# Kernel optimization log

Measured on AMD Instinct MI355X. Metric: run time of the kernel, lower is better.

## Reference

```python
import jax, jax.numpy as jnp
import numpy as np

EMBED_DIM = 1024
NUM_HEADS = 16
HEAD_DIM = EMBED_DIM // NUM_HEADS
SCALE = HEAD_DIM ** -0.5
B, N = 2, 2048


def setup_inputs() -> dict:
    key = jax.random.key(0)
    ks = jax.random.split(key, 18)
    s = 1.0 / np.sqrt(EMBED_DIM)
    inp = {
        'x': jax.random.normal(ks[0], (B, N, EMBED_DIM), jnp.float32),
        'context': jax.random.normal(ks[1], (B, N, EMBED_DIM), jnp.float32),
    }
    names = ['q', 'k', 'v', 'o', 'cq', 'ck', 'cv']
    for i, nm in enumerate(names):
        inp['W' + nm] = jax.random.normal(ks[2 + 2 * i], (EMBED_DIM, EMBED_DIM), jnp.float32) * s
        inp['b' + nm] = jax.random.normal(ks[3 + 2 * i], (EMBED_DIM,), jnp.float32) * s
    return inp


def _linear(x, W, b):
    # torch nn.Linear: x @ W.T + b, W is [out, in]
    return jnp.einsum('bnc,oc->bno', x, W) + b


def reference(x, context, Wq, bq, Wk, bk, Wv, bv, Wo, bo, Wcq, bcq, Wck, bck, Wcv, bcv):
    Bsz, Nseq, C = x.shape
    # self-attention with head split
    def split(t):
        return t.reshape(Bsz, Nseq, NUM_HEADS, HEAD_DIM).transpose(0, 2, 1, 3)  # [B,H,N,D]
    q = split(_linear(x, Wq, bq))
    k = split(_linear(x, Wk, bk))
    v = split(_linear(x, Wv, bv))
    scores = jnp.einsum('bhnd,bhmd->bhnm', q, k) * SCALE  # [B,H,N,N]
    attn = jax.nn.softmax(scores, axis=-1)  # dropout is identity in eval
    out = jnp.einsum('bhnm,bhmd->bhnd', attn, v)
    out = out.transpose(0, 2, 1, 3).reshape(Bsz, Nseq, C)
    attn_output = _linear(out, Wo, bo)
    # cross-attention branch: NO head split (faithful to original)
    cq = _linear(attn_output, Wcq, bcq)  # [B,N,C]
    ck = _linear(context, Wck, bck)      # [B,M,C]
    cv = _linear(context, Wcv, bcv)      # [B,M,C]
    cscores = jnp.einsum('bnc,bmc->bnm', cq, ck) * SCALE  # [B,N,M]
    cattn = jax.nn.softmax(cscores, axis=-1)
    cross_out = jnp.einsum('bnm,bmc->bnc', cattn, cv)
    return attn_output + cross_out
```

## Files before the change

kernel.cpp:

```cpp
#include <hip/hip_runtime.h>
#include <stdint.h>

typedef __attribute__((ext_vector_type(8))) short short8;
typedef __attribute__((ext_vector_type(4))) float f32x4;
typedef unsigned short u16;
typedef unsigned int u32;

#define SCALE 0.125f

__device__ __forceinline__ u16 f2bf(float f) {
  u32 u = __builtin_bit_cast(u32, f);
  u32 r = (u + 0x7FFFu + ((u >> 16) & 1u)) >> 16;
  return (u16)r;
}
__device__ __forceinline__ u16 f2bf_fast(float f) {
  return (u16)((__builtin_bit_cast(u32, f) + 0x8000u) >> 16);
}
__device__ __forceinline__ float bf2f(u16 h) {
  u32 u = ((u32)h) << 16;
  return __builtin_bit_cast(float, u);
}

__device__ __forceinline__ void gload16(const void* g, void* l) {
  __builtin_amdgcn_global_load_lds(
      (const __attribute__((address_space(1))) u32*)g,
      (__attribute__((address_space(3))) u32*)l, 16, 0, 0);
}

#define MFMA16(a, b, c) __builtin_amdgcn_mfma_f32_16x16x32_bf16((a), (b), (c), 0, 0, 0)

__global__ void fill_f32(float* __restrict__ p, float v, int n) {
  int i = blockIdx.x * 256 + threadIdx.x;
  if (i < n) p[i] = v;
}

__global__ void cvt_f32_bf16_s(const float* __restrict__ src, u16* __restrict__ dst,
                               int n, float s) {
  int i = (blockIdx.x * 256 + threadIdx.x) * 4;
  if (i >= n) return;
  float4 v = *(const float4*)(src + i);
  u32* d = (u32*)(dst + i);
  d[0] = (u32)f2bf(v.x * s) | ((u32)f2bf(v.y * s) << 16);
  d[1] = (u32)f2bf(v.z * s) | ((u32)f2bf(v.w * s) << 16);
}

__global__ void copy_scale_f32(const float* __restrict__ s, float* __restrict__ d,
                               int n, float sc) {
  int i = blockIdx.x * 256 + threadIdx.x;
  if (i < n) d[i] = s[i] * sc;
}

template <int MODE>
__global__ __launch_bounds__(512) void gemm_nt(
    const u16* __restrict__ A, int64_t lda, int64_t sAz,
    const u16* __restrict__ B, int64_t ldb, int64_t sBz,
    void* __restrict__ Cv, int64_t ldc, int64_t sCz, u16* __restrict__ C2,
    const float* __restrict__ bias, const float* __restrict__ biasR,
    float alpha, int K)
{
  __shared__ u16 sA[128 * 64];
  __shared__ u16 sB[128 * 64];
  const int tid = threadIdx.x;
  const int lane = tid & 63, w = tid >> 6, g = lane >> 4, c = lane & 15;
  const int wr = w >> 1, wc = w & 1;
  const int64_t m0 = (int64_t)blockIdx.y * 128, n0 = (int64_t)blockIdx.x * 128;
  A += (int64_t)blockIdx.z * sAz;
  B += (int64_t)blockIdx.z * sBz;

  f32x4 acc[2][4] = {};

  int sL[2];
  const u16* gA[2];
  const u16* gB[2];
#pragma unroll
  for (int i = 0; i < 2; ++i) {
    int s = tid + i * 512;
    int row = s >> 3;
    sL[i] = s * 16;
    int scol = ((sL[i] ^ ((row & 7) << 4)) & 127) >> 1;
    gA[i] = A + (m0 + row) * lda + scol;
    gB[i] = B + (n0 + row) * ldb + scol;
  }

  for (int k0 = 0; k0 < K; k0 += 64) {
    __syncthreads();
#pragma unroll
    for (int i = 0; i < 2; ++i) {
      gload16(gA[i] + k0, (char*)sA + sL[i]);
      gload16(gB[i] + k0, (char*)sB + sL[i]);
    }
    __syncthreads();
#pragma unroll
    for (int kk = 0; kk < 2; ++kk) {
      short8 af[2], bf[4];
#pragma unroll
      for (int m = 0; m < 2; ++m) {
        int row = wr * 32 + m * 16 + c;
        int off = (row * 128 + kk * 64 + g * 16) ^ ((row & 7) << 4);
        af[m] = *(const short8*)((const char*)sA + off);
      }
#pragma unroll
      for (int n = 0; n < 4; ++n) {
        int row = wc * 64 + n * 16 + c;
        int off = (row * 128 + kk * 64 + g * 16) ^ ((row & 7) << 4);
        bf[n] = *(const short8*)((const char*)sB + off);
      }
#pragma unroll
      for (int m = 0; m < 2; ++m)
#pragma unroll
        for (int n = 0; n < 4; ++n)
          acc[m][n] = MFMA16(af[m], bf[n], acc[m][n]);
    }
  }

#pragma unroll
  for (int m = 0; m < 2; ++m) {
#pragma unroll
    for (int n = 0; n < 4; ++n) {
#pragma unroll
      for (int j = 0; j < 4; ++j) {
        int64_t r = m0 + wr * 32 + m * 16 + g * 4 + j;
        int64_t col = n0 + wc * 64 + n * 16 + c;
        float v = acc[m][n][j] * alpha;
        if (bias) v += bias[col];
        if (biasR) v += biasR[r];
        v = fminf(fmaxf(v, -1.0e4f), 1.0e4f);
        int64_t idx = (int64_t)blockIdx.z * sCz + r * ldc + col;
        if (MODE == 0) ((u16*)Cv)[idx] = f2bf(v);
        else if (MODE == 1) { ((float*)Cv)[idx] = v; C2[idx] = f2bf(v); }
        else ((float*)Cv)[idx] += v;
      }
    }
  }
}

__global__ __launch_bounds__(512) void flash_attn(const u16* __restrict__ QKV,
                                                  u16* __restrict__ O)
{
  __shared__ u16 sK[64 * 64];
  __shared__ u16 sV[64 * 64];
  __shared__ u16 sP[8][16 * 64];
  const int tid = threadIdx.x;
  const int lane = tid & 63, w = tid >> 6, g = lane >> 4, c = lane & 15;
  const int h = blockIdx.y, b = blockIdx.z;
  const int64_t rowbase = (int64_t)b * 2048;
  const int q0 = blockIdx.x * 128 + w * 16;

  short8 aq[2];
  {
    const u16* qp = QKV + (rowbase + q0 + c) * 3072 + h * 64 + g * 8;
    aq[0] = *(const short8*)qp;
    aq[1] = *(const short8*)(qp + 32);
  }
  const u16* Kbase = QKV + rowbase * 3072 + 1024 + h * 64;
  const u16* Vbase = QKV + rowbase * 3072 + 2048 + h * 64;

  float lrun[4] = {0.f, 0.f, 0.f, 0.f};
  f32x4 accO[4] = {};

  const int krow = tid >> 3;
  const int kL = tid * 16;
  const int kcol = ((kL ^ ((krow & 7) << 4)) & 127) >> 1;
  const u16* gK = Kbase + (int64_t)krow * 3072 + kcol;
  const int vkp = tid & 31, vd8 = ((tid >> 5) & 7) * 8;
  const u16* gV = Vbase + (int64_t)(2 * vkp) * 3072 + vd8;

  short8 r0{}, r1{};
  if (tid < 256) {
    r0 = *(const short8*)(gV);
    r1 = *(const short8*)(gV + 3072);
  }

  for (int kt = 0; kt < 2048; kt += 64) {
    __syncthreads();
    gload16(gK + (int64_t)kt * 3072, (char*)sK + kL);
    if (tid < 256) {
#pragma unroll
      for (int i = 0; i < 8; ++i) {
        int d = vd8 + i;
        int off = (d * 128 + vkp * 4) ^ ((d & 7) << 4);
        u32 val = (u32)(u16)r0[i] | ((u32)(u16)r1[i] << 16);
        *(u32*)((char*)sV + off) = val;
      }
    }
    __syncthreads();
    if (kt + 64 < 2048 && tid < 256) {
      r0 = *(const short8*)(gV + (int64_t)(kt + 64) * 3072);
      r1 = *(const short8*)(gV + (int64_t)(kt + 64) * 3072 + 3072);
    }

    f32x4 s[4];
#pragma unroll
    for (int kb = 0; kb < 4; ++kb) {
      int row = kb * 16 + c;
      int off = (row * 128 + g * 16) ^ ((row & 7) << 4);
      short8 bk0 = *(const short8*)((const char*)sK + off);
      short8 bk1 = *(const short8*)((const char*)sK + (off ^ 64));
      f32x4 z = {0.f, 0.f, 0.f, 0.f};
      z = MFMA16(aq[0], bk0, z);
      z = MFMA16(aq[1], bk1, z);
      s[kb] = z;
    }
    u16* sPw = &sP[w][0];
#pragma unroll
    for (int kb = 0; kb < 4; ++kb)
#pragma unroll
      for (int j = 0; j < 4; ++j) {
        float pv = __expf(s[kb][j] - 8.f);
        lrun[j] += pv;
        int r = g * 4 + j, cc = kb * 16 + c;
        int off = (r * 128 + cc * 2) ^ ((r & 7) << 4);
        *(u16*)((char*)sPw + off) = f2bf_fast(pv);
      }
    __syncthreads();
    short8 ap[2];
#pragma unroll
    for (int ks = 0; ks < 2; ++ks) {
      int off = (c * 128 + ks * 64 + g * 16) ^ ((c & 7) << 4);
      ap[ks] = *(const short8*)((const char*)sPw + off);
    }
#pragma unroll
    for (int d = 0; d < 4; ++d) {
#pragma unroll
      for (int ks = 0; ks < 2; ++ks) {
        int vr = d * 16 + c;
        int off = (vr * 128 + ks * 64 + g * 16) ^ ((vr & 7) << 4);
        short8 bv = *(const short8*)((const char*)sV + off);
        accO[d] = MFMA16(ap[ks], bv, accO[d]);
      }
    }
  }
#pragma unroll
  for (int msk = 1; msk <= 8; msk <<= 1)
#pragma unroll
    for (int j = 0; j < 4; ++j)
      lrun[j] += __shfl_xor(lrun[j], msk);
#pragma unroll
  for (int j = 0; j < 4; ++j) {
    float inv = 1.f / fmaxf(lrun[j], 1e-30f);
    int64_t q = rowbase + q0 + g * 4 + j;
#pragma unroll
    for (int d = 0; d < 4; ++d)
      O[q * 1024 + h * 64 + d * 16 + c] = f2bf(accO[d][j] * inv);
  }
}

__global__ __launch_bounds__(256) void softmax_bf16(u16* __restrict__ S) {
  __shared__ float red[256];
  const int64_t row = blockIdx.x;
  u16* p = S + row * 2048;
  const int t = threadIdx.x;
  short8 raw = *(const short8*)(p + t * 8);
  float vv[8];
#pragma unroll
  for (int i = 0; i < 8; ++i) vv[i] = bf2f((u16)raw[i]);
  float m = vv[0];
#pragma unroll
  for (int i = 1; i < 8; ++i) m = fmaxf(m, vv[i]);
  red[t] = m;
  __syncthreads();
  for (int s = 128; s > 0; s >>= 1) {
    if (t < s) red[t] = fmaxf(red[t], red[t + s]);
    __syncthreads();
  }
  m = red[0];
  __syncthreads();
  float e[8], sum = 0.f;
#pragma unroll
  for (int i = 0; i < 8; ++i) { e[i] = __expf(vv[i] - m); sum += e[i]; }
  red[t] = sum;
  __syncthreads();
  for (int s = 128; s > 0; s >>= 1) {
    if (t < s) red[t] += red[t + s];
    __syncthreads();
  }
  sum = red[0];
  float inv = 1.f / fmaxf(sum, 1e-30f);
  short8 outv;
#pragma unroll
  for (int i = 0; i < 8; ++i) outv[i] = (short)f2bf_fast(e[i] * inv);
  *(short8*)(p + t * 8) = outv;
}

extern "C" void kernel_launch(void* const* d_in, const int* in_sizes, int n_in,
                              void* d_out, int out_size, void* d_ws, size_t ws_size,
                              hipStream_t stream) {
  float* out = (float*)d_out;

  bool ok = (n_in == 16) && (in_sizes[0] == 4194304) && (in_sizes[1] == 4194304);
  for (int i = 2; i < 16 && ok; i += 2)
    ok = (in_sizes[i] == 1048576) && (in_sizes[i + 1] == 1024);
  if (!ok) {
    fill_f32<<<(out_size + 255) / 256, 256, 0, stream>>>(out, 1000.0f, out_size);
    return;
  }

  const float* x   = (const float*)d_in[0];
  const float* ctx = (const float*)d_in[1];
  const float* Wq  = (const float*)d_in[2];   const float* bq  = (const float*)d_in[3];
  const float* Wk  = (const float*)d_in[4];   const float* bk  = (const float*)d_in[5];
  const float* Wv  = (const float*)d_in[6];   const float* bv  = (const float*)d_in[7];
  const float* Wo  = (const float*)d_in[8];   const float* bo  = (const float*)d_in[9];
  const float* Wcq = (const float*)d_in[10];  const float* bcq = (const float*)d_in[11];
  const float* Wck = (const float*)d_in[12];  const float* bck = (const float*)d_in[13];
  const float* Wcv = (const float*)d_in[14];  const float* bcv = (const float*)d_in[15];

  const size_t ARENA = 56635392;
  if (ws_size < ARENA) {
    fill_f32<<<(out_size + 255) / 256, 256, 0, stream>>>(out, 12345.0f, out_size);
    return;
  }
  char* ws = (char*)d_ws;
  u16* QKV   = (u16*)(ws + 0);
  u16* aob   = (u16*)(ws + 0);
  u16* cq    = (u16*)(ws + 8388608);
  u16* ckb   = (u16*)(ws + 16777216);
  u16* xb    = (u16*)(ws + 25165824);
  u16* Obuf  = (u16*)(ws + 25165824);
  u16* cvT   = (u16*)(ws + 25165824);
  u16* cb    = (u16*)(ws + 33554432);
  u16* Wqkvb = (u16*)(ws + 41943040);
  float* bqkv = (float*)(ws + 48234496);
  u16* SP    = (u16*)(ws + 33554432);
  u16* Wob   = (u16*)(ws + 48246784);
  u16* Wcqb  = (u16*)(ws + 50343936);
  u16* Wckb  = (u16*)(ws + 52441088);
  u16* Wcvb  = (u16*)(ws + 54538240);

  const int MEL = 4194304, WEL = 1048576;
  cvt_f32_bf16_s<<<MEL / 1024, 256, 0, stream>>>(x, xb, MEL, 1.f);
  cvt_f32_bf16_s<<<MEL / 1024, 256, 0, stream>>>(ctx, cb, MEL, 1.f);
  cvt_f32_bf16_s<<<WEL / 1024, 256, 0, stream>>>(Wq, Wqkvb, WEL, SCALE);
  cvt_f32_bf16_s<<<WEL / 1024, 256, 0, stream>>>(Wk, Wqkvb + WEL, WEL, 1.f);
  cvt_f32_bf16_s<<<WEL / 1024, 256, 0, stream>>>(Wv, Wqkvb + 2 * WEL, WEL, 1.f);
  cvt_f32_bf16_s<<<WEL / 1024, 256, 0, stream>>>(Wo, Wob, WEL, 1.f);
  cvt_f32_bf16_s<<<WEL / 1024, 256, 0, stream>>>(Wcq, Wcqb, WEL, 1.f);
  cvt_f32_bf16_s<<<WEL / 1024, 256, 0, stream>>>(Wck, Wckb, WEL, 1.f);
  cvt_f32_bf16_s<<<WEL / 1024, 256, 0, stream>>>(Wcv, Wcvb, WEL, 1.f);
  copy_scale_f32<<<4, 256, 0, stream>>>(bq, bqkv, 1024, SCALE);
  copy_scale_f32<<<4, 256, 0, stream>>>(bk, bqkv + 1024, 1024, 1.f);
  copy_scale_f32<<<4, 256, 0, stream>>>(bv, bqkv + 2048, 1024, 1.f);

  gemm_nt<0><<<dim3(24, 32, 1), 512, 0, stream>>>(xb, 1024, 0, Wqkvb, 1024, 0,
      QKV, 3072, 0, nullptr, bqkv, nullptr, 1.f, 1024);
  flash_attn<<<dim3(16, 16, 2), 512, 0, stream>>>(QKV, Obuf);
  gemm_nt<1><<<dim3(8, 32, 1), 512, 0, stream>>>(Obuf, 1024, 0, Wob, 1024, 0,
      out, 1024, 0, aob, bo, nullptr, 1.f, 1024);
  gemm_nt<0><<<dim3(8, 32, 1), 512, 0, stream>>>(aob, 1024, 0, Wcqb, 1024, 0,
      cq, 1024, 0, nullptr, bcq, nullptr, 1.f, 1024);
  gemm_nt<0><<<dim3(8, 32, 1), 512, 0, stream>>>(cb, 1024, 0, Wckb, 1024, 0,
      ckb, 1024, 0, nullptr, bck, nullptr, 1.f, 1024);
  gemm_nt<0><<<dim3(16, 8, 2), 512, 0, stream>>>(Wcvb, 1024, 0,
      cb, 1024, 2048LL * 1024, cvT, 2048, 1024LL * 2048, nullptr,
      nullptr, bcv, 1.f, 1024);
  gemm_nt<0><<<dim3(16, 16, 2), 512, 0, stream>>>(cq, 1024, 2048LL * 1024,
      ckb, 1024, 2048LL * 1024, SP, 2048, 2048LL * 2048, nullptr,
      nullptr, nullptr, SCALE, 1024);
  softmax_bf16<<<4096, 256, 0, stream>>>(SP);
  gemm_nt<2><<<dim3(8, 16, 2), 512, 0, stream>>>(SP, 2048, 2048LL * 2048,
      cvT, 2048, 1024LL * 2048, out, 1024, 2048LL * 1024, nullptr,
      nullptr, nullptr, 1.f, 2048);
}
```

Before: 306.9 us.

## Double-buffer GEMM LDS tiles and merge weight/bias conversion launches

The GEMM kernel now keeps two LDS buffers for the A and B tiles. It issues the global-to-LDS loads for the next K tile before computing on the current one, and drops to one barrier per iteration, so load latency can overlap with MFMA work. Separately, the seven weight conversion launches and three bias copy launches are merged into one prep_weights kernel and one prep_bias kernel to cut launch overhead. Doubling LDS to 64KB per block may lower occupancy.

```diff
diff --git a/kernel.cpp b/kernel.cpp
--- a/kernel.cpp
+++ b/kernel.cpp
@@ -44,10 +44,41 @@
   d[1] = (u32)f2bf(v.z * s) | ((u32)f2bf(v.w * s) << 16);
 }
 
-__global__ void copy_scale_f32(const float* __restrict__ s, float* __restrict__ d,
-                               int n, float sc) {
+__global__ void prep_weights(const float* __restrict__ Wq, const float* __restrict__ Wk,
+                             const float* __restrict__ Wv, const float* __restrict__ Wo,
+                             const float* __restrict__ Wcq, const float* __restrict__ Wck,
+                             const float* __restrict__ Wcv,
+                             u16* __restrict__ Wqkvb, u16* __restrict__ Wob,
+                             u16* __restrict__ Wcqb, u16* __restrict__ Wckb,
+                             u16* __restrict__ Wcvb) {
+  const int WEL = 1048576;
+  int blk = blockIdx.x;
+  int which = blk >> 10;
+  int i = ((blk & 1023) * 256 + threadIdx.x) * 4;
+  const float* s;
+  u16* d;
+  float sc = 1.f;
+  switch (which) {
+    case 0: s = Wq;  d = Wqkvb;            sc = SCALE; break;
+    case 1: s = Wk;  d = Wqkvb + WEL;      break;
+    case 2: s = Wv;  d = Wqkvb + 2 * WEL;  break;
+    case 3: s = Wo;  d = Wob;              break;
+    case 4: s = Wcq; d = Wcqb;             break;
+    case 5: s = Wck; d = Wckb;             break;
+    default: s = Wcv; d = Wcvb;            break;
+  }
+  float4 v = *(const float4*)(s + i);
+  u32* dd = (u32*)(d + i);
+  dd[0] = (u32)f2bf(v.x * sc) | ((u32)f2bf(v.y * sc) << 16);
+  dd[1] = (u32)f2bf(v.z * sc) | ((u32)f2bf(v.w * sc) << 16);
+}
+
+__global__ void prep_bias(const float* __restrict__ bq, const float* __restrict__ bk,
+                          const float* __restrict__ bv, float* __restrict__ bqkv) {
   int i = blockIdx.x * 256 + threadIdx.x;
-  if (i < n) d[i] = s[i] * sc;
+  if (i < 1024) bqkv[i] = bq[i] * SCALE;
+  else if (i < 2048) bqkv[i] = bk[i - 1024];
+  else bqkv[i] = bv[i - 2048];
 }
 
 template <int MODE>
@@ -58,8 +89,8 @@
     const float* __restrict__ bias, const float* __restrict__ biasR,
     float alpha, int K)
 {
-  __shared__ u16 sA[128 * 64];
-  __shared__ u16 sB[128 * 64];
+  __shared__ u16 sA[2][128 * 64];
+  __shared__ u16 sB[2][128 * 64];
   const int tid = threadIdx.x;
   const int lane = tid & 63, w = tid >> 6, g = lane >> 4, c = lane & 15;
   const int wr = w >> 1, wc = w & 1;
@@ -82,14 +113,25 @@
     gB[i] = B + (n0 + row) * ldb + scol;
   }
 
-  for (int k0 = 0; k0 < K; k0 += 64) {
-    __syncthreads();
-#pragma unroll
-    for (int i = 0; i < 2; ++i) {
-      gload16(gA[i] + k0, (char*)sA + sL[i]);
-      gload16(gB[i] + k0, (char*)sB + sL[i]);
-    }
-    __syncthreads();
+#pragma unroll
+  for (int i = 0; i < 2; ++i) {
+    gload16(gA[i], (char*)sA[0] + sL[i]);
+    gload16(gB[i], (char*)sB[0] + sL[i]);
+  }
+  __syncthreads();
+
+  const int nt = K >> 6;
+  for (int t = 0; t < nt; ++t) {
+    const int cur = t & 1;
+    if (t + 1 < nt) {
+      const int nxt = cur ^ 1;
+      const int64_t koff = (int64_t)(t + 1) * 64;
+#pragma unroll
+      for (int i = 0; i < 2; ++i) {
+        gload16(gA[i] + koff, (char*)sA[nxt] + sL[i]);
+        gload16(gB[i] + koff, (char*)sB[nxt] + sL[i]);
+      }
+    }
 #pragma unroll
     for (int kk = 0; kk < 2; ++kk) {
       short8 af[2], bf[4];
@@ -97,13 +139,13 @@
       for (int m = 0; m < 2; ++m) {
         int row = wr * 32 + m * 16 + c;
         int off = (row * 128 + kk * 64 + g * 16) ^ ((row & 7) << 4);
-        af[m] = *(const short8*)((const char*)sA + off);
+        af[m] = *(const short8*)((const char*)sA[cur] + off);
       }
 #pragma unroll
       for (int n = 0; n < 4; ++n) {
         int row = wc * 64 + n * 16 + c;
         int off = (row * 128 + kk * 64 + g * 16) ^ ((row & 7) << 4);
-        bf[n] = *(const short8*)((const char*)sB + off);
+        bf[n] = *(const short8*)((const char*)sB[cur] + off);
       }
 #pragma unroll
       for (int m = 0; m < 2; ++m)
@@ -111,6 +153,7 @@
         for (int n = 0; n < 4; ++n)
           acc[m][n] = MFMA16(af[m], bf[n], acc[m][n]);
     }
+    __syncthreads();
   }
 
 #pragma unroll
@@ -327,19 +370,12 @@
   u16* Wckb  = (u16*)(ws + 52441088);
   u16* Wcvb  = (u16*)(ws + 54538240);
 
-  const int MEL = 4194304, WEL = 1048576;
+  const int MEL = 4194304;
   cvt_f32_bf16_s<<<MEL / 1024, 256, 0, stream>>>(x, xb, MEL, 1.f);
   cvt_f32_bf16_s<<<MEL / 1024, 256, 0, stream>>>(ctx, cb, MEL, 1.f);
-  cvt_f32_bf16_s<<<WEL / 1024, 256, 0, stream>>>(Wq, Wqkvb, WEL, SCALE);
-  cvt_f32_bf16_s<<<WEL / 1024, 256, 0, stream>>>(Wk, Wqkvb + WEL, WEL, 1.f);
-  cvt_f32_bf16_s<<<WEL / 1024, 256, 0, stream>>>(Wv, Wqkvb + 2 * WEL, WEL, 1.f);
-  cvt_f32_bf16_s<<<WEL / 1024, 256, 0, stream>>>(Wo, Wob, WEL, 1.f);
-  cvt_f32_bf16_s<<<WEL / 1024, 256, 0, stream>>>(Wcq, Wcqb, WEL, 1.f);
-  cvt_f32_bf16_s<<<WEL / 1024, 256, 0, stream>>>(Wck, Wckb, WEL, 1.f);
-  cvt_f32_bf16_s<<<WEL / 1024, 256, 0, stream>>>(Wcv, Wcvb, WEL, 1.f);
-  copy_scale_f32<<<4, 256, 0, stream>>>(bq, bqkv, 1024, SCALE);
-  copy_scale_f32<<<4, 256, 0, stream>>>(bk, bqkv + 1024, 1024, 1.f);
-  copy_scale_f32<<<4, 256, 0, stream>>>(bv, bqkv + 2048, 1024, 1.f);
+  prep_weights<<<7 * 1024, 256, 0, stream>>>(Wq, Wk, Wv, Wo, Wcq, Wck, Wcv,
+      Wqkvb, Wob, Wcqb, Wckb, Wcvb);
+  prep_bias<<<12, 256, 0, stream>>>(bq, bk, bv, bqkv);
 
   gemm_nt<0><<<dim3(24, 32, 1), 512, 0, stream>>>(xb, 1024, 0, Wqkvb, 1024, 0,
       QKV, 3072, 0, nullptr, bqkv, nullptr, 1.f, 1024);
```

Measured after the change: 286.3 us, median of 2. 1.07x faster.
